# Optimization experiments

Measured on AMD Instinct MI355X. Metric: run time of the kernel, lower is better.

Reference implementation:

```python
import jax, jax.numpy as jnp
import numpy as np

LN_EPS = 1e-6  # flax.linen.LayerNorm default


def setup_inputs() -> dict:
    key = jax.random.key(0)
    ks = jax.random.split(key, 16)
    N_TOT, M = 32768, 12            # total atoms, neighbors per atom
    ORIG, EDGE = 92, 41             # CGCNN atom / edge feature dims
    F, H, L = 128, 256, 3           # atom_fea_len, h_fea_len, n_conv

    def w(k, shape, fan_in):
        return jax.random.normal(k, shape, dtype=jnp.float32) / np.sqrt(fan_in).astype(np.float32)

    return {
        "atom_fea": jax.random.normal(ks[0], (N_TOT, ORIG), dtype=jnp.float32),
        "nbr_fea": jax.random.normal(ks[1], (N_TOT, M, EDGE), dtype=jnp.float32),
        "nbr_fea_idx": jax.random.randint(ks[2], (N_TOT, M), 0, N_TOT),
        # embedding Dense
        "W_embed": w(ks[3], (ORIG, F), ORIG), "b_embed": jnp.zeros((F,), jnp.float32),
        # per-conv-layer stacked params [L, ...]
        "W_center": w(ks[4], (L, F, F), F), "b_center": jnp.zeros((L, F), jnp.float32),
        "W_nbr": w(ks[5], (L, F, F), F), "b_nbr": jnp.zeros((L, F), jnp.float32),
        "W_edge": w(ks[6], (L, EDGE, F), EDGE), "b_edge": jnp.zeros((L, F), jnp.float32),
        "W_gate": w(ks[7], (L, F, F), F), "b_gate": jnp.zeros((L, F), jnp.float32),
        "W_mag": w(ks[8], (L, F, F), F), "b_mag": jnp.zeros((L, F), jnp.float32),
        "ln_scale": jnp.ones((L, F), jnp.float32), "ln_bias": jnp.zeros((L, F), jnp.float32),
        # readout: Dense(h) -> softplus -> Dense(1)
        "W_h": w(ks[9], (F, H), F), "b_h": jnp.zeros((H,), jnp.float32),
        "W_out": w(ks[10], (H, 1), H), "b_out": jnp.zeros((1,), jnp.float32),
        "batch_size": 128,
        "n_atoms_per_crystal": 256,
    }


def _layernorm(x, scale, bias):
    mu = jnp.mean(x, axis=-1, keepdims=True)
    var = jnp.mean(jnp.square(x - mu), axis=-1, keepdims=True)
    return (x - mu) * jax.lax.rsqrt(var + LN_EPS) * scale + bias


def reference(atom_fea, nbr_fea, nbr_fea_idx, W_embed, b_embed,
              W_center, b_center, W_nbr, b_nbr, W_edge, b_edge,
              W_gate, b_gate, W_mag, b_mag, ln_scale, ln_bias,
              W_h, b_h, W_out, b_out, batch_size, n_atoms_per_crystal):
    n_conv = W_center.shape[0]
    x = atom_fea @ W_embed + b_embed                       # [N, F]
    for i in range(n_conv):
        atom_nbr = jnp.take(x, nbr_fea_idx, axis=0)        # [N, M, F] gather
        # Dense on tiled center == Dense on center then broadcast
        phi_c = (x @ W_center[i] + b_center[i])[:, None, :]   # [N, 1, F]
        phi_n = atom_nbr @ W_nbr[i] + b_nbr[i]                # [N, M, F]
        phi_e = nbr_fea @ W_edge[i] + b_edge[i]               # [N, M, F]
        inter = phi_c * phi_n * phi_e                          # [N, M, F]
        gate = jax.nn.sigmoid(inter @ W_gate[i] + b_gate[i])
        mag = jax.nn.softplus(inter @ W_mag[i] + b_mag[i])
        nbr_sumed = jnp.sum(gate * mag, axis=1)               # [N, F]
        x = x + _layernorm(nbr_sumed, ln_scale[i], ln_bias[i])
    E_site = jax.nn.softplus(x @ W_h + b_h) @ W_out + b_out   # [N, 1]
    return jnp.sum(E_site.reshape(batch_size, n_atoms_per_crystal), axis=1, keepdims=True)  # [B, 1]
```

## Files before the change

### kernel.cpp

```cpp
#include <hip/hip_runtime.h>
#include <math.h>

#define N_TOT 32768
#define M_NBR 12
#define ORIG  92
#define EDGE  41
#define FD    128
#define HD    256
#define APC   256
#define NCRY  128

#define STR   136
#define WF_PER_LAYER 73728
#define WF_EMBED     12288
#define WF_H         32768

typedef __attribute__((ext_vector_type(8))) short bf16x8;
typedef __attribute__((ext_vector_type(4))) float f32x4;

__device__ __forceinline__ short f2bf(float f) {
    union { float f; unsigned u; } v; v.f = f;
    unsigned r = v.u + 0x7fffu + ((v.u >> 16) & 1u);
    return (short)(r >> 16);
}
__device__ __forceinline__ float bf2f(short s) {
    union { unsigned u; float f; } v; v.u = ((unsigned)(unsigned short)s) << 16;
    return v.f;
}
__device__ __forceinline__ float softplus_f(float x) {
    return fmaxf(x, 0.0f) + __logf(1.0f + __expf(-fabsf(x)));
}
__device__ __forceinline__ float sigmoid_f(float x) {
    return 1.0f / (1.0f + __expf(-x));
}

__global__ __launch_bounds__(256) void swizzle_kernel(
    const float* __restrict__ Wc_all, const float* __restrict__ Wn_all,
    const float* __restrict__ We_all, const float* __restrict__ Wg_all,
    const float* __restrict__ Wm_all, const float* __restrict__ W_embed,
    const float* __restrict__ W_h, short* __restrict__ dst_all)
{
    int gid = blockIdx.x * 256 + threadIdx.x;
    if (gid >= 33280) return;
    const float* W; short* dst; int K_real, fid, stride, l, nt, kt;
    if (gid < 27648) {
        int layer = gid / 9216;
        int rem = gid - layer * 9216;
        short* dbase = dst_all + layer * WF_PER_LAYER;
        if (rem < 2048)      { W = Wc_all + layer * 16384; dst = dbase;         K_real = 128; fid = rem; }
        else if (rem < 4096) { W = Wn_all + layer * 16384; dst = dbase + 16384; K_real = 128; fid = rem - 2048; }
        else if (rem < 5120) { W = We_all + layer * 5248;  dst = dbase + 32768; K_real = 41;  fid = rem - 4096; }
        else if (rem < 7168) { W = Wg_all + layer * 16384; dst = dbase + 40960; K_real = 128; fid = rem - 5120; }
        else                 { W = Wm_all + layer * 16384; dst = dbase + 57344; K_real = 128; fid = rem - 7168; }
        stride = 128; l = fid & 63; nt = (fid >> 6) & 7; kt = fid >> 9;
    } else if (gid < 29184) {
        fid = gid - 27648;
        W = W_embed; dst = dst_all + 3 * WF_PER_LAYER; K_real = ORIG; stride = 128;
        l = fid & 63; nt = (fid >> 6) & 7; kt = fid >> 9;
    } else {
        fid = gid - 29184;
        W = W_h; dst = dst_all + 3 * WF_PER_LAYER + WF_EMBED; K_real = 128; stride = 256;
        l = fid & 63; nt = (fid >> 6) & 15; kt = fid >> 10;
    }
    int n = nt * 16 + (l & 15), kb = kt * 32 + (l >> 4) * 8;
    bf16x8 v;
    #pragma unroll
    for (int j = 0; j < 8; ++j) {
        int k = kb + j;
        v[j] = (k < K_real) ? f2bf(W[k * stride + n]) : (short)0;
    }
    *(bf16x8*)(dst + fid * 8) = v;
}

__global__ __launch_bounds__(256) void embed_mfma_kernel(
    const float* __restrict__ atom_fea, const short* __restrict__ wef,
    const float* __restrict__ b, float* __restrict__ x, short* __restrict__ xbf)
{
    const int tid = threadIdx.x;
    const int w = tid >> 6, lane = tid & 63;
    const int q = lane >> 4, m = lane & 15;
    const int a0 = blockIdx.x * 64;
    const int arow = a0 + w * 16 + m;

    bf16x8 aA[3];
    const float* ap = atom_fea + (long)arow * ORIG;
    #pragma unroll
    for (int kt = 0; kt < 3; ++kt) {
        const int kb = kt * 32 + q * 8;
        bf16x8 v;
        if (kb + 7 < ORIG) {
            const float4 u0 = *(const float4*)(ap + kb);
            const float4 u1 = *(const float4*)(ap + kb + 4);
            v[0]=f2bf(u0.x); v[1]=f2bf(u0.y); v[2]=f2bf(u0.z); v[3]=f2bf(u0.w);
            v[4]=f2bf(u1.x); v[5]=f2bf(u1.y); v[6]=f2bf(u1.z); v[7]=f2bf(u1.w);
        } else {
            #pragma unroll
            for (int j = 0; j < 8; ++j) {
                const int k = kb + j;
                v[j] = (k < ORIG) ? f2bf(ap[k]) : (short)0;
            }
        }
        aA[kt] = v;
    }

    #pragma unroll
    for (int nt = 0; nt < 8; ++nt) {
        f32x4 C = {0.f, 0.f, 0.f, 0.f};
        #pragma unroll
        for (int kt = 0; kt < 3; ++kt)
            C = __builtin_amdgcn_mfma_f32_16x16x32_bf16(
                    aA[kt], *(const bf16x8*)(wef + ((kt * 8 + nt) * 64 + lane) * 8), C, 0, 0, 0);
        const int col = nt * 16 + m;
        const float bv = b[col];
        #pragma unroll
        for (int r = 0; r < 4; ++r) {
            const long n = a0 + w * 16 + q * 4 + r;
            const float val = C[r] + bv;
            x[n * FD + col] = val;
            xbf[n * FD + col] = f2bf(val);
        }
    }
}

__global__ __launch_bounds__(256) void conv_mfma_kernel(
    const float* __restrict__ x_in, const short* __restrict__ xbf_in,
    float* __restrict__ x_out, short* __restrict__ xbf_out,
    const float* __restrict__ nbr_fea, const int* __restrict__ nbr_idx,
    const short* __restrict__ wf,
    const float* __restrict__ bc, const float* __restrict__ bn,
    const float* __restrict__ be, const float* __restrict__ bg,
    const float* __restrict__ bm,
    const float* __restrict__ lns, const float* __restrict__ lnb)
{
    __shared__ short inter_s[192 * STR];
    __shared__ float phic_s[16 * 132];
    __shared__ int   idx_s[192];

    const int tid = threadIdx.x;
    const int w = tid >> 6, lane = tid & 63;
    const int q = lane >> 4, m = lane & 15;
    const int a0 = blockIdx.x * 16;
    const long r0 = (long)a0 * M_NBR;

    const short* Wc = wf;
    const short* Wn = wf + 16384;
    const short* We = wf + 32768;
    const short* Wg = wf + 40960;
    const short* Wm = wf + 57344;

    if (tid < 192) idx_s[tid] = nbr_idx[r0 + tid];

    {
        bf16x8 aC[4];
        #pragma unroll
        for (int kt = 0; kt < 4; ++kt)
            aC[kt] = *(const bf16x8*)(xbf_in + ((long)(a0 + m) << 7) + kt * 32 + q * 8);
        #pragma unroll
        for (int ii = 0; ii < 2; ++ii) {
            const int nt = w * 2 + ii;
            f32x4 C = {0.f, 0.f, 0.f, 0.f};
            #pragma unroll
            for (int kt = 0; kt < 4; ++kt)
                C = __builtin_amdgcn_mfma_f32_16x16x32_bf16(
                        aC[kt], *(const bf16x8*)(Wc + ((kt * 8 + nt) * 64 + lane) * 8), C, 0, 0, 0);
            const int col = nt * 16 + m;
            const float bcv = bc[col];
            #pragma unroll
            for (int r = 0; r < 4; ++r)
                phic_s[(q * 4 + r) * 132 + col] = C[r] + bcv;
        }
    }
    __syncthreads();

    bf16x8 aN[3][4];
    #pragma unroll
    for (int i = 0; i < 3; ++i) {
        const int row = (w * 3 + i) * 16 + m;
        const long g = (long)idx_s[row] << 7;
        #pragma unroll
        for (int kt = 0; kt < 4; ++kt)
            aN[i][kt] = *(const bf16x8*)(xbf_in + g + kt * 32 + q * 8);
    }
    bf16x8 aE[3][2];
    #pragma unroll
    for (int i = 0; i < 3; ++i) {
        const int row = (w * 3 + i) * 16 + m;
        const float* ep = nbr_fea + (r0 + row) * EDGE;
        bf16x8 e0, e1;
        #pragma unroll
        for (int j = 0; j < 8; ++j) e0[j] = f2bf(ep[q * 8 + j]);
        #pragma unroll
        for (int j = 0; j < 8; ++j) e1[j] = 0;
        if (q == 0) {
            #pragma unroll
            for (int j = 0; j < 8; ++j) e1[j] = f2bf(ep[32 + j]);
        } else if (q == 1) {
            e1[0] = f2bf(ep[40]);
        }
        aE[i][0] = e0; aE[i][1] = e1;
    }

    #pragma unroll
    for (int nt = 0; nt < 8; ++nt) {
        f32x4 Cn[3], Ce[3];
        #pragma unroll
        for (int i = 0; i < 3; ++i) { Cn[i] = (f32x4){0.f,0.f,0.f,0.f}; Ce[i] = (f32x4){0.f,0.f,0.f,0.f}; }
        #pragma unroll
        for (int kt = 0; kt < 4; ++kt) {
            const bf16x8 bfr = *(const bf16x8*)(Wn + ((kt * 8 + nt) * 64 + lane) * 8);
            #pragma unroll
            for (int i = 0; i < 3; ++i)
                Cn[i] = __builtin_amdgcn_mfma_f32_16x16x32_bf16(aN[i][kt], bfr, Cn[i], 0, 0, 0);
        }
        #pragma unroll
        for (int kt = 0; kt < 2; ++kt) {
            const bf16x8 efr = *(const bf16x8*)(We + ((kt * 8 + nt) * 64 + lane) * 8);
            #pragma unroll
            for (int i = 0; i < 3; ++i)
                Ce[i] = __builtin_amdgcn_mfma_f32_16x16x32_bf16(aE[i][kt], efr, Ce[i], 0, 0, 0);
        }
        const int col = nt * 16 + m;
        const float bnv = bn[col], bev = be[col];
        #pragma unroll
        for (int i = 0; i < 3; ++i) {
            const int rb = (w * 3 + i) * 16 + q * 4;
            #pragma unroll
            for (int r = 0; r < 4; ++r) {
                const int row = rb + r;
                const int atom = row / 12;
                const float iv = phic_s[atom * 132 + col] * (Cn[i][r] + bnv) * (Ce[i][r] + bev);
                inter_s[row * STR + col] = f2bf(iv);
            }
        }
    }

    bf16x8 aI[3][4];
    #pragma unroll
    for (int i = 0; i < 3; ++i) {
        const int row = (w * 3 + i) * 16 + m;
        #pragma unroll
        for (int kt = 0; kt < 4; ++kt)
            aI[i][kt] = *(const bf16x8*)(inter_s + row * STR + kt * 32 + q * 8);
    }

    #pragma unroll
    for (int nt = 0; nt < 8; ++nt) {
        f32x4 Cg[3], Cm[3];
        #pragma unroll
        for (int i = 0; i < 3; ++i) { Cg[i] = (f32x4){0.f,0.f,0.f,0.f}; Cm[i] = (f32x4){0.f,0.f,0.f,0.f}; }
        #pragma unroll
        for (int kt = 0; kt < 4; ++kt) {
            const bf16x8 gfr = *(const bf16x8*)(Wg + ((kt * 8 + nt) * 64 + lane) * 8);
            const bf16x8 mfr = *(const bf16x8*)(Wm + ((kt * 8 + nt) * 64 + lane) * 8);
            #pragma unroll
            for (int i = 0; i < 3; ++i) {
                Cg[i] = __builtin_amdgcn_mfma_f32_16x16x32_bf16(aI[i][kt], gfr, Cg[i], 0, 0, 0);
                Cm[i] = __builtin_amdgcn_mfma_f32_16x16x32_bf16(aI[i][kt], mfr, Cm[i], 0, 0, 0);
            }
        }
        const int col = nt * 16 + m;
        const float bgv = bg[col], bmv = bm[col];
        #pragma unroll
        for (int i = 0; i < 3; ++i) {
            const int rb = (w * 3 + i) * 16 + q * 4;
            #pragma unroll
            for (int r = 0; r < 4; ++r) {
                const float g = sigmoid_f(Cg[i][r] + bgv);
                const float s = softplus_f(Cm[i][r] + bmv);
                inter_s[(rb + r) * STR + col] = f2bf(g * s);
            }
        }
    }
    __syncthreads();

    {
        const int a = tid >> 4;
        const int cg = tid & 15;
        float s8[8];
        #pragma unroll
        for (int j = 0; j < 8; ++j) s8[j] = 0.f;
        #pragma unroll
        for (int nb = 0; nb < 12; ++nb) {
            const bf16x8 p = *(const bf16x8*)(inter_s + (a * 12 + nb) * STR + cg * 8);
            #pragma unroll
            for (int j = 0; j < 8; ++j) s8[j] += bf2f(p[j]);
        }
        float lsum = 0.f, lsq = 0.f;
        #pragma unroll
        for (int j = 0; j < 8; ++j) { lsum += s8[j]; lsq += s8[j] * s8[j]; }
        #pragma unroll
        for (int off = 1; off < 16; off <<= 1) {
            lsum += __shfl_xor(lsum, off, 64);
            lsq  += __shfl_xor(lsq,  off, 64);
        }
        const float mu = lsum * (1.0f / FD);
        float var = lsq * (1.0f / FD) - mu * mu;
        var = fmaxf(var, 0.0f);
        const float inv = rsqrtf(var + 1e-6f);
        const long xb = ((long)(a0 + a) << 7) + cg * 8;
        float o[8]; bf16x8 ob;
        #pragma unroll
        for (int j = 0; j < 8; ++j) {
            const int col = cg * 8 + j;
            const float y = (s8[j] - mu) * inv * lns[col] + lnb[col];
            const float v = x_in[xb + j] + y;
            o[j] = v; ob[j] = f2bf(v);
        }
        *(float4*)(x_out + xb)     = make_float4(o[0], o[1], o[2], o[3]);
        *(float4*)(x_out + xb + 4) = make_float4(o[4], o[5], o[6], o[7]);
        *(bf16x8*)(xbf_out + xb)   = ob;
    }
}

__global__ __launch_bounds__(256) void readout_mfma_kernel(
    const short* __restrict__ xbf, const short* __restrict__ whf,
    const float* __restrict__ bh, const float* __restrict__ Wo,
    const float* __restrict__ bo, float* __restrict__ out)
{
    const int tid = threadIdx.x;
    const int w = tid >> 6, lane = tid & 63;
    const int q = lane >> 4, m = lane & 15;
    const int a0 = blockIdx.x * 64;
    const int arow = a0 + w * 16 + m;

    bf16x8 aX[4];
    #pragma unroll
    for (int kt = 0; kt < 4; ++kt)
        aX[kt] = *(const bf16x8*)(xbf + ((long)arow << 7) + kt * 32 + q * 8);

    float e[4] = {0.f, 0.f, 0.f, 0.f};
    #pragma unroll
    for (int nt = 0; nt < 16; ++nt) {
        f32x4 C = {0.f, 0.f, 0.f, 0.f};
        #pragma unroll
        for (int kt = 0; kt < 4; ++kt)
            C = __builtin_amdgcn_mfma_f32_16x16x32_bf16(
                    aX[kt], *(const bf16x8*)(whf + ((kt * 16 + nt) * 64 + lane) * 8), C, 0, 0, 0);
        const int col = nt * 16 + m;
        const float bhv = bh[col], wov = Wo[col];
        #pragma unroll
        for (int r = 0; r < 4; ++r)
            e[r] += softplus_f(C[r] + bhv) * wov;
    }
    float esum = e[0] + e[1] + e[2] + e[3];
    #pragma unroll
    for (int off = 32; off > 0; off >>= 1)
        esum += __shfl_xor(esum, off, 64);
    if (lane == 0)
        atomicAdd(&out[a0 / APC], esum + 16.0f * bo[0]);
}

__global__ void zero_out_kernel(float* __restrict__ out) {
    if (threadIdx.x < NCRY) out[threadIdx.x] = 0.0f;
}

extern "C" void kernel_launch(void* const* d_in, const int* in_sizes, int n_in,
                              void* d_out, int out_size, void* d_ws, size_t ws_size,
                              hipStream_t stream) {
    const float* atom_fea = (const float*)d_in[0];
    const float* nbr_fea  = (const float*)d_in[1];
    const int*   nbr_idx  = (const int*)d_in[2];
    const float* W_embed  = (const float*)d_in[3];
    const float* b_embed  = (const float*)d_in[4];
    const float* W_center = (const float*)d_in[5];
    const float* b_center = (const float*)d_in[6];
    const float* W_nbr    = (const float*)d_in[7];
    const float* b_nbr    = (const float*)d_in[8];
    const float* W_edge   = (const float*)d_in[9];
    const float* b_edge   = (const float*)d_in[10];
    const float* W_gate   = (const float*)d_in[11];
    const float* b_gate   = (const float*)d_in[12];
    const float* W_mag    = (const float*)d_in[13];
    const float* b_mag    = (const float*)d_in[14];
    const float* ln_scale = (const float*)d_in[15];
    const float* ln_bias  = (const float*)d_in[16];
    const float* W_h      = (const float*)d_in[17];
    const float* b_h      = (const float*)d_in[18];
    const float* W_out    = (const float*)d_in[19];
    const float* b_out    = (const float*)d_in[20];

    float* out = (float*)d_out;
    const size_t NX = (size_t)N_TOT * FD;
    float* xA = (float*)d_ws;
    float* xB = xA + NX;
    short* xbfA = (short*)(xB + NX);
    short* xbfB = xbfA + NX;
    short* wfrag = xbfB + NX;

    swizzle_kernel<<<130, 256, 0, stream>>>(W_center, W_nbr, W_edge, W_gate, W_mag,
                                            W_embed, W_h, wfrag);
    embed_mfma_kernel<<<N_TOT / 64, 256, 0, stream>>>(
        atom_fea, wfrag + 3 * WF_PER_LAYER, b_embed, xA, xbfA);

    const float* xi = xA; float* xo = xB;
    const short* xbi = xbfA; short* xbo = xbfB;
    for (int l = 0; l < 3; ++l) {
        conv_mfma_kernel<<<N_TOT / 16, 256, 0, stream>>>(
            xi, xbi, xo, xbo, nbr_fea, nbr_idx,
            wfrag + (size_t)l * WF_PER_LAYER,
            b_center + (size_t)l * FD, b_nbr + (size_t)l * FD,
            b_edge + (size_t)l * FD, b_gate + (size_t)l * FD,
            b_mag + (size_t)l * FD,
            ln_scale + (size_t)l * FD, ln_bias + (size_t)l * FD);
        const float* tf = xo; xo = (float*)xi; xi = tf;
        const short* tb = xbo; xbo = (short*)xbi; xbi = tb;
    }

    zero_out_kernel<<<1, 128, 0, stream>>>(out);
    readout_mfma_kernel<<<N_TOT / 64, 256, 0, stream>>>(
        xbi, wfrag + 3 * WF_PER_LAYER + WF_EMBED, b_h, W_out, b_out, out);
}
```

Before: 465.8 us.

## Pre-convert edge features to bf16 and XOR-swizzle LDS in conv kernel

A new prep kernel converts nbr_fea once into a padded bf16 layout, so each of the three conv layers reads it with vector loads instead of re-reading and converting fp32 data. The conv kernel now keeps neighbor indices in registers and issues the gather and edge loads before the center GEMM. It stores phi_c as bf16, applies an XOR swizzle instead of padding to the intermediate LDS tile, and drops a barrier that is unneeded because each wave reads only the rows it wrote. It also adds a 3-block occupancy hint and vectorizes the residual load. The cost is an extra pass over nbr_fea plus a workspace buffer, and phi_c now carries bf16 precision loss.

```diff
diff --git a/kernel.cpp b/kernel.cpp
--- a/kernel.cpp
+++ b/kernel.cpp
@@ -10,7 +10,7 @@
 #define APC   256
 #define NCRY  128
 
-#define STR   136
+#define ESTR  48
 #define WF_PER_LAYER 73728
 #define WF_EMBED     12288
 #define WF_H         32768
@@ -72,6 +72,22 @@
     *(bf16x8*)(dst + fid * 8) = v;
 }
 
+__global__ __launch_bounds__(256) void edge_prep_kernel(
+    const float* __restrict__ nbr_fea, short* __restrict__ edge_frag)
+{
+    const long R = (long)N_TOT * M_NBR;
+    const long gid = (long)blockIdx.x * 256 + threadIdx.x;
+    const long row = gid / 6;
+    const int c = (int)(gid - row * 6);
+    if (row >= R) return;
+    const float* src = nbr_fea + row * EDGE + c * 8;
+    bf16x8 v;
+    #pragma unroll
+    for (int j = 0; j < 8; ++j)
+        v[j] = (c * 8 + j < EDGE) ? f2bf(src[j]) : (short)0;
+    *(bf16x8*)(edge_frag + row * ESTR + c * 8) = v;
+}
+
 __global__ __launch_bounds__(256) void embed_mfma_kernel(
     const float* __restrict__ atom_fea, const short* __restrict__ wef,
     const float* __restrict__ b, float* __restrict__ x, short* __restrict__ xbf)
@@ -122,19 +138,18 @@
     }
 }
 
-__global__ __launch_bounds__(256) void conv_mfma_kernel(
+__global__ __launch_bounds__(256, 3) void conv_mfma_kernel(
     const float* __restrict__ x_in, const short* __restrict__ xbf_in,
     float* __restrict__ x_out, short* __restrict__ xbf_out,
-    const float* __restrict__ nbr_fea, const int* __restrict__ nbr_idx,
+    const short* __restrict__ edge_frag, const int* __restrict__ nbr_idx,
     const short* __restrict__ wf,
     const float* __restrict__ bc, const float* __restrict__ bn,
     const float* __restrict__ be, const float* __restrict__ bg,
     const float* __restrict__ bm,
     const float* __restrict__ lns, const float* __restrict__ lnb)
 {
-    __shared__ short inter_s[192 * STR];
-    __shared__ float phic_s[16 * 132];
-    __shared__ int   idx_s[192];
+    __shared__ short inter_s[192 * 128];
+    __shared__ short phic_s[16 * 136];
 
     const int tid = threadIdx.x;
     const int w = tid >> 6, lane = tid & 63;
@@ -148,7 +163,34 @@
     const short* Wg = wf + 40960;
     const short* Wm = wf + 57344;
 
-    if (tid < 192) idx_s[tid] = nbr_idx[r0 + tid];
+    int idx[3];
+    #pragma unroll
+    for (int i = 0; i < 3; ++i)
+        idx[i] = nbr_idx[r0 + (w * 3 + i) * 16 + m];
+
+    bf16x8 aE[3][2];
+    #pragma unroll
+    for (int i = 0; i < 3; ++i) {
+        const long erow = r0 + (w * 3 + i) * 16 + m;
+        aE[i][0] = *(const bf16x8*)(edge_frag + erow * ESTR + q * 8);
+        if (q < 2) {
+            aE[i][1] = *(const bf16x8*)(edge_frag + erow * ESTR + 32 + q * 8);
+        } else {
+            bf16x8 z;
+            #pragma unroll
+            for (int j = 0; j < 8; ++j) z[j] = 0;
+            aE[i][1] = z;
+        }
+    }
+
+    bf16x8 aN[3][4];
+    #pragma unroll
+    for (int i = 0; i < 3; ++i) {
+        const long g = (long)idx[i] << 7;
+        #pragma unroll
+        for (int kt = 0; kt < 4; ++kt)
+            aN[i][kt] = *(const bf16x8*)(xbf_in + g + kt * 32 + q * 8);
+    }
 
     {
         bf16x8 aC[4];
@@ -167,38 +209,10 @@
             const float bcv = bc[col];
             #pragma unroll
             for (int r = 0; r < 4; ++r)
-                phic_s[(q * 4 + r) * 132 + col] = C[r] + bcv;
+                phic_s[(q * 4 + r) * 136 + col] = f2bf(C[r] + bcv);
         }
     }
     __syncthreads();
-
-    bf16x8 aN[3][4];
-    #pragma unroll
-    for (int i = 0; i < 3; ++i) {
-        const int row = (w * 3 + i) * 16 + m;
-        const long g = (long)idx_s[row] << 7;
-        #pragma unroll
-        for (int kt = 0; kt < 4; ++kt)
-            aN[i][kt] = *(const bf16x8*)(xbf_in + g + kt * 32 + q * 8);
-    }
-    bf16x8 aE[3][2];
-    #pragma unroll
-    for (int i = 0; i < 3; ++i) {
-        const int row = (w * 3 + i) * 16 + m;
-        const float* ep = nbr_fea + (r0 + row) * EDGE;
-        bf16x8 e0, e1;
-        #pragma unroll
-        for (int j = 0; j < 8; ++j) e0[j] = f2bf(ep[q * 8 + j]);
-        #pragma unroll
-        for (int j = 0; j < 8; ++j) e1[j] = 0;
-        if (q == 0) {
-            #pragma unroll
-            for (int j = 0; j < 8; ++j) e1[j] = f2bf(ep[32 + j]);
-        } else if (q == 1) {
-            e1[0] = f2bf(ep[40]);
-        }
-        aE[i][0] = e0; aE[i][1] = e1;
-    }
 
     #pragma unroll
     for (int nt = 0; nt < 8; ++nt) {
@@ -220,6 +234,7 @@
                 Ce[i] = __builtin_amdgcn_mfma_f32_16x16x32_bf16(aE[i][kt], efr, Ce[i], 0, 0, 0);
         }
         const int col = nt * 16 + m;
+        const int chunkL = col >> 3, sub = col & 7;
         const float bnv = bn[col], bev = be[col];
         #pragma unroll
         for (int i = 0; i < 3; ++i) {
@@ -228,8 +243,9 @@
             for (int r = 0; r < 4; ++r) {
                 const int row = rb + r;
                 const int atom = row / 12;
-                const float iv = phic_s[atom * 132 + col] * (Cn[i][r] + bnv) * (Ce[i][r] + bev);
-                inter_s[row * STR + col] = f2bf(iv);
+                const float pc = bf2f(phic_s[(atom & 15) * 136 + col]);
+                const float iv = pc * (Cn[i][r] + bnv) * (Ce[i][r] + bev);
+                inter_s[row * 128 + ((chunkL ^ (row & 15)) << 3) + sub] = f2bf(iv);
             }
         }
     }
@@ -240,7 +256,7 @@
         const int row = (w * 3 + i) * 16 + m;
         #pragma unroll
         for (int kt = 0; kt < 4; ++kt)
-            aI[i][kt] = *(const bf16x8*)(inter_s + row * STR + kt * 32 + q * 8);
+            aI[i][kt] = *(const bf16x8*)(inter_s + row * 128 + (((kt * 4 + q) ^ m) << 3));
     }
 
     #pragma unroll
@@ -259,19 +275,20 @@
             }
         }
         const int col = nt * 16 + m;
+        const int chunkL = col >> 3, sub = col & 7;
         const float bgv = bg[col], bmv = bm[col];
         #pragma unroll
         for (int i = 0; i < 3; ++i) {
             const int rb = (w * 3 + i) * 16 + q * 4;
             #pragma unroll
             for (int r = 0; r < 4; ++r) {
+                const int row = rb + r;
                 const float g = sigmoid_f(Cg[i][r] + bgv);
                 const float s = softplus_f(Cm[i][r] + bmv);
-                inter_s[(rb + r) * STR + col] = f2bf(g * s);
+                inter_s[row * 128 + ((chunkL ^ (row & 15)) << 3) + sub] = f2bf(g * s);
             }
         }
     }
-    __syncthreads();
 
     {
         const int a = tid >> 4;
@@ -281,7 +298,8 @@
         for (int j = 0; j < 8; ++j) s8[j] = 0.f;
         #pragma unroll
         for (int nb = 0; nb < 12; ++nb) {
-            const bf16x8 p = *(const bf16x8*)(inter_s + (a * 12 + nb) * STR + cg * 8);
+            const int row = a * 12 + nb;
+            const bf16x8 p = *(const bf16x8*)(inter_s + row * 128 + ((cg ^ (row & 15)) << 3));
             #pragma unroll
             for (int j = 0; j < 8; ++j) s8[j] += bf2f(p[j]);
         }
@@ -298,12 +316,15 @@
         var = fmaxf(var, 0.0f);
         const float inv = rsqrtf(var + 1e-6f);
         const long xb = ((long)(a0 + a) << 7) + cg * 8;
+        const float4 xr0 = *(const float4*)(x_in + xb);
+        const float4 xr1 = *(const float4*)(x_in + xb + 4);
+        const float xr[8] = {xr0.x, xr0.y, xr0.z, xr0.w, xr1.x, xr1.y, xr1.z, xr1.w};
         float o[8]; bf16x8 ob;
         #pragma unroll
         for (int j = 0; j < 8; ++j) {
             const int col = cg * 8 + j;
             const float y = (s8[j] - mu) * inv * lns[col] + lnb[col];
-            const float v = x_in[xb + j] + y;
+            const float v = xr[j] + y;
             o[j] = v; ob[j] = f2bf(v);
         }
         *(float4*)(x_out + xb)     = make_float4(o[0], o[1], o[2], o[3]);
@@ -386,9 +407,11 @@
     short* xbfA = (short*)(xB + NX);
     short* xbfB = xbfA + NX;
     short* wfrag = xbfB + NX;
+    short* edge_frag = wfrag + 266240;
 
     swizzle_kernel<<<130, 256, 0, stream>>>(W_center, W_nbr, W_edge, W_gate, W_mag,
                                             W_embed, W_h, wfrag);
+    edge_prep_kernel<<<9216, 256, 0, stream>>>(nbr_fea, edge_frag);
     embed_mfma_kernel<<<N_TOT / 64, 256, 0, stream>>>(
         atom_fea, wfrag + 3 * WF_PER_LAYER, b_embed, xA, xbfA);
 
@@ -396,7 +419,7 @@
     const short* xbi = xbfA; short* xbo = xbfB;
     for (int l = 0; l < 3; ++l) {
         conv_mfma_kernel<<<N_TOT / 16, 256, 0, stream>>>(
-            xi, xbi, xo, xbo, nbr_fea, nbr_idx,
+            xi, xbi, xo, xbo, edge_frag, nbr_idx,
             wfrag + (size_t)l * WF_PER_LAYER,
             b_center + (size_t)l * FD, b_nbr + (size_t)l * FD,
             b_edge + (size_t)l * FD, b_gate + (size_t)l * FD,
```

Result: slower. 741.8 us (+59.2%).
